# Kernel optimization log

Hardware: AMD Instinct MI355X
Metric: run time of the kernel (lower is better)

## Reference

```python
import jax, jax.numpy as jnp
import numpy as np

H = 64  # GRU hidden size


def _gru_layer(x, Wih, Whh, bih, bhh):
    """PyTorch-semantics GRU layer. x: [B,T,I] -> [B,T,H].
    r = sig(Wir x + bir + Whr h + bhr); z = sig(...); n = tanh(Win x + bin + r*(Whn h + bhn))
    h' = (1-z)*n + z*h. Gate order in stacked weights: r, z, n."""
    xg = jnp.einsum('bti,gi->btg', x, Wih) + bih  # [B,T,3H], precomputed input projections

    def step(h, xg_t):
        hg = h @ Whh.T + bhh  # [B,3H]
        xr, xz, xn = jnp.split(xg_t, 3, axis=-1)
        hr, hz, hn = jnp.split(hg, 3, axis=-1)
        r = jax.nn.sigmoid(xr + hr)
        z = jax.nn.sigmoid(xz + hz)
        n = jnp.tanh(xn + r * hn)
        h_new = (1.0 - z) * n + z * h
        return h_new, h_new

    h0 = jnp.zeros((x.shape[0], H), x.dtype)
    _, ys = jax.lax.scan(step, h0, jnp.swapaxes(xg, 0, 1))  # scan over time
    return jnp.swapaxes(ys, 0, 1)  # [B,T,H]


def _gru_stack4(x, Wih0, Wih, Whh, bih, bhh):
    # layer 0 has its own input width; layers 1..3 take H->H. Inter-layer dropout
    # (p=0.2) is inference-disabled.
    y = _gru_layer(x, Wih0, Whh[0], bih[0], bhh[0])
    for l in range(3):
        y = _gru_layer(y, Wih[l], Whh[l + 1], bih[l + 1], bhh[l + 1])
    return y


def _bn_eval(x, gamma, beta, mean, var, eps=1e-5):
    return gamma * (x - mean) * jax.lax.rsqrt(var + eps) + beta


def setup_inputs() -> dict:
    key = jax.random.key(0)
    ks = jax.random.split(key, 32)
    B, T = 2048, 256
    d = {}
    d['sentiment_seq'] = jax.random.normal(ks[0], (B, T), jnp.float32)
    d['price_seq'] = jax.random.normal(ks[1], (B, T, 4), jnp.float32)
    w = lambda k, s: jax.random.normal(k, s, jnp.float32) * 0.1
    d['s_Wih0'] = w(ks[2], (192, 1)); d['s_Wih'] = w(ks[3], (3, 192, 64))
    d['s_Whh'] = w(ks[4], (4, 192, 64)); d['s_bih'] = w(ks[5], (4, 192)); d['s_bhh'] = w(ks[6], (4, 192))
    d['p_Wih0'] = w(ks[7], (192, 4)); d['p_Wih'] = w(ks[8], (3, 192, 64))
    d['p_Whh'] = w(ks[9], (4, 192, 64)); d['p_bih'] = w(ks[10], (4, 192)); d['p_bhh'] = w(ks[11], (4, 192))
    d['fc1_W'] = w(ks[12], (128, 128)); d['fc1_b'] = w(ks[13], (128,))
    d['bn1_gamma'] = jax.random.uniform(ks[14], (128,), jnp.float32, 0.5, 1.5)
    d['bn1_beta'] = w(ks[15], (128,)); d['bn1_mean'] = w(ks[16], (128,))
    d['bn1_var'] = jax.random.uniform(ks[17], (128,), jnp.float32, 0.5, 1.5)
    d['fc2_W'] = w(ks[18], (128, 128)); d['fc2_b'] = w(ks[19], (128,))
    d['bn2_gamma'] = jax.random.uniform(ks[20], (128,), jnp.float32, 0.5, 1.5)
    d['bn2_beta'] = w(ks[21], (128,)); d['bn2_mean'] = w(ks[22], (128,))
    d['bn2_var'] = jax.random.uniform(ks[23], (128,), jnp.float32, 0.5, 1.5)
    d['fc3_W'] = w(ks[24], (2, 128)); d['fc3_b'] = w(ks[25], (2,))
    return d


def reference(sentiment_seq, price_seq,
              s_Wih0, s_Wih, s_Whh, s_bih, s_bhh,
              p_Wih0, p_Wih, p_Whh, p_bih, p_bhh,
              fc1_W, fc1_b, bn1_gamma, bn1_beta, bn1_mean, bn1_var,
              fc2_W, fc2_b, bn2_gamma, bn2_beta, bn2_mean, bn2_var,
              fc3_W, fc3_b):
    # input_size[0] == 1 -> unsqueeze last dim (as in the torch module)
    s = sentiment_seq[..., None]                         # [B,T,1]
    s_out = _gru_stack4(s, s_Wih0, s_Wih, s_Whh, s_bih, s_bhh)
    p_out = _gru_stack4(price_seq, p_Wih0, p_Wih, p_Whh, p_bih, p_bhh)
    x = jnp.concatenate([s_out[:, -1, :], p_out[:, -1, :]], axis=1)  # [B,128]
    x = x @ fc1_W.T + fc1_b
    x = jax.nn.relu(_bn_eval(x, bn1_gamma, bn1_beta, bn1_mean, bn1_var))  # dropout off (eval)
    x = x @ fc2_W.T + fc2_b
    x = jax.nn.relu(_bn_eval(x, bn2_gamma, bn2_beta, bn2_mean, bn2_var))
    return x @ fc3_W.T + fc3_b  # [B,2] logits
```

## Files before the change

### kernel.cpp

```cpp
#include <hip/hip_runtime.h>

namespace {

constexpr int BB = 2048;
constexpr int TT = 256;
constexpr float L2E = 1.4426950408889634f;

typedef __attribute__((ext_vector_type(8))) short bf8;
typedef __attribute__((ext_vector_type(4))) float f4;
typedef __attribute__((ext_vector_type(2))) unsigned int u32x2;

#define MFMA16(a, b, c) __builtin_amdgcn_mfma_f32_16x16x32_bf16((a), (b), (c), 0, 0, 0)

__device__ __forceinline__ unsigned short f2bf_rne(float f) {
  unsigned int x = __float_as_uint(f);
  return (unsigned short)((x + 0x7fffu + ((x >> 16) & 1u)) >> 16);
}
__device__ __forceinline__ void mk_hilo(float v, short& hi, short& lo) {
  unsigned int u = __float_as_uint(v);
  hi = (short)(u >> 16);
  float r = v - __uint_as_float(u & 0xffff0000u);
  lo = (short)(__float_as_uint(r) >> 16);
}

__device__ __forceinline__ void waitq(const unsigned* c, unsigned tgt) {
  while (__hip_atomic_load(c, __ATOMIC_ACQUIRE, __HIP_MEMORY_SCOPE_WORKGROUP) < tgt) {}
}

__global__ __launch_bounds__(1024, 4) void gru_all(
    const float* __restrict__ xs, const float* __restrict__ xp,
    const float* __restrict__ W0s, const float* __restrict__ W0p,
    const float* __restrict__ Wihs, const float* __restrict__ Wihp,
    const float* __restrict__ Whhs, const float* __restrict__ Whhp,
    const float* __restrict__ bihs, const float* __restrict__ bihp,
    const float* __restrict__ bhhs, const float* __restrict__ bhhp,
    float* __restrict__ hlast) {
  const int tid = threadIdx.x;
  const int Wv = tid >> 6, lane = tid & 63;
  const int g = Wv >> 2, w = Wv & 3;
  const int n15 = lane & 15, q = lane >> 4;
  const int blk = blockIdx.x, stack = blk >> 7;
  const int b0 = (blk & 127) * 16;

  const float* Wh = (stack ? Whhp : Whhs) + (size_t)g * 192 * 64;
  const float* bi = (stack ? bihp : bihs) + g * 192;
  const float* bh = (stack ? bhhp : bhhs) + g * 192;
  const float* Wx = (stack ? Wihp : Wihs) + (size_t)(g - 1) * 192 * 64;

  __shared__ unsigned short hb[4][4][8][16][8];
  __shared__ unsigned qdone[4];

  for (int e = tid; e < 4 * 4 * 8 * 16 * 8; e += 1024)
    ((unsigned short*)hb)[e] = 0;
  if (tid < 4) qdone[tid] = 0;
  __syncthreads();

  const int mrow = 16 * w + n15;
  const int mu = 16 * w + 4 * q;
  const int fr_w = 2 * w + (q >> 1);
  const int eo_w = (q & 1) * 4;

  const float gsc[3] = {L2E, L2E, 2.f * L2E};

  bf8 whh_[3][2];
  #pragma unroll
  for (int i = 0; i < 3; ++i) {
    #pragma unroll
    for (int kt = 0; kt < 2; ++kt) {
      const float* ph_ = Wh + (size_t)(i * 64 + mrow) * 64 + kt * 32 + q * 8;
      f4 ha = *(const f4*)ph_, hc = *(const f4*)(ph_ + 4);
      bf8 h2;
      #pragma unroll
      for (int j = 0; j < 8; ++j)
        h2[j] = (short)f2bf_rne(gsc[i] * ((j < 4) ? ha[j] : hc[j - 4]));
      whh_[i][kt] = h2;
    }
  }
  bf8 wxh_[3][2];
  if (g >= 1) {
    #pragma unroll
    for (int i = 0; i < 3; ++i) {
      #pragma unroll
      for (int kt = 0; kt < 2; ++kt) {
        const float* px_ = Wx + (size_t)(i * 64 + mrow) * 64 + kt * 32 + q * 8;
        f4 xa = *(const f4*)px_, xc = *(const f4*)(px_ + 4);
        bf8 h1;
        #pragma unroll
        for (int j = 0; j < 8; ++j)
          h1[j] = (short)f2bf_rne(gsc[i] * ((j < 4) ? xa[j] : xc[j - 4]));
        wxh_[i][kt] = h1;
      }
    }
  } else {
    const float* W0 = stack ? W0p : W0s;
    #pragma unroll
    for (int i = 0; i < 3; ++i) {
      bf8 a;
      #pragma unroll
      for (int j = 0; j < 8; ++j) a[j] = 0;
      if (q == 0) {
        if (stack) {
          #pragma unroll
          for (int d = 0; d < 4; ++d) {
            short hi, lo;
            mk_hilo(gsc[i] * W0[(size_t)(i * 64 + mrow) * 4 + d], hi, lo);
            a[d] = hi; a[4 + d] = lo;
          }
        } else {
          short hi, lo; mk_hilo(gsc[i] * W0[i * 64 + mrow], hi, lo);
          a[0] = hi; a[1] = hi; a[4] = lo; a[5] = lo;
        }
      }
      wxh_[i][0] = a; wxh_[i][1] = a;
    }
  }

  f4 bR, bZ, bNx, bNh;
  #pragma unroll
  for (int r = 0; r < 4; ++r) {
    bR[r]  = L2E * (bi[mu + r] + bh[mu + r]);
    bZ[r]  = L2E * (bi[64 + mu + r] + bh[64 + mu + r]);
    bNx[r] = 2.f * L2E * bi[128 + mu + r];
    bNh[r] = 2.f * L2E * bh[128 + mu + r];
  }
  f4 h = {0.f, 0.f, 0.f, 0.f};

  const size_t xrow = (size_t)(b0 + n15);
  float px0 = 0.f, px1 = 0.f, px2 = 0.f, px3 = 0.f;
  if (g == 0) {
    if (stack) { f4 t4 = *(const f4*)(xp + xrow * TT * 4); px0 = t4[0]; px1 = t4[1]; px2 = t4[2]; px3 = t4[3]; }
    else       { px0 = xs[xrow * TT]; }
  }

#define GRU_BODY(S)                                                            \
  {                                                                            \
    constexpr int SW = (S + 1) & 3;                                            \
    f4 aR = bR, aZ = bZ, aNx = bNx, aNh = bNh;                                 \
    if (g == 0) {                                                              \
      bf8 xq;                                                                  \
      _Pragma("unroll") for (int j = 0; j < 8; ++j) xq[j] = 0;                 \
      if (q == 0) {                                                            \
        if (stack) {                                                           \
          short a0 = (short)f2bf_rne(px0), a1 = (short)f2bf_rne(px1);          \
          short a2 = (short)f2bf_rne(px2), a3 = (short)f2bf_rne(px3);          \
          xq[0] = a0; xq[1] = a1; xq[2] = a2; xq[3] = a3;                      \
          xq[4] = a0; xq[5] = a1; xq[6] = a2; xq[7] = a3;                      \
        } else {                                                               \
          unsigned short xh = f2bf_rne(px0);                                   \
          float xf = __uint_as_float((unsigned)xh << 16);                      \
          unsigned short xl = f2bf_rne(px0 - xf);                              \
          xq[0] = (short)xh; xq[1] = (short)xl;                                \
          xq[4] = (short)xh; xq[5] = (short)xl;                                \
        }                                                                      \
      }                                                                        \
      __builtin_amdgcn_s_setprio(1);                                           \
      aR  = MFMA16(wxh_[0][0], xq, aR);                                        \
      aZ  = MFMA16(wxh_[1][0], xq, aZ);                                        \
      aNx = MFMA16(wxh_[2][0], xq, aNx);                                       \
      __builtin_amdgcn_s_setprio(0);                                           \
      if (tc + 1 < TT) {                                                       \
        if (stack) { f4 t4 = *(const f4*)(xp + (xrow * TT + tc + 1) * 4);      \
                     px0 = t4[0]; px1 = t4[1]; px2 = t4[2]; px3 = t4[3]; }     \
        else       { px0 = xs[xrow * TT + tc + 1]; }                           \
      }                                                                        \
    } else {                                                                   \
      waitq(&qdone[g - 1], 4u * (unsigned)(tc + 1));                           \
      bf8 xc0 = *(const bf8*)&hb[g - 1][SW][q][n15][0];                        \
      bf8 xc1 = *(const bf8*)&hb[g - 1][SW][4 + q][n15][0];                    \
      __builtin_amdgcn_s_setprio(1);                                           \
      aR  = MFMA16(wxh_[0][0], xc0, aR);  aR  = MFMA16(wxh_[0][1], xc1, aR);   \
      aZ  = MFMA16(wxh_[1][0], xc0, aZ);  aZ  = MFMA16(wxh_[1][1], xc1, aZ);   \
      aNx = MFMA16(wxh_[2][0], xc0, aNx); aNx = MFMA16(wxh_[2][1], xc1, aNx);  \
      __builtin_amdgcn_s_setprio(0);                                           \
    }                                                                          \
    waitq(&qdone[g], 4u * (unsigned)tc);                                       \
    bf8 hh0 = *(const bf8*)&hb[g][S][q][n15][0];                               \
    bf8 hh1 = *(const bf8*)&hb[g][S][4 + q][n15][0];                           \
    __builtin_amdgcn_s_setprio(1);                                             \
    aR  = MFMA16(whh_[0][0], hh0, aR);  aR  = MFMA16(whh_[0][1], hh1, aR);     \
    aZ  = MFMA16(whh_[1][0], hh0, aZ);  aZ  = MFMA16(whh_[1][1], hh1, aZ);     \
    aNh = MFMA16(whh_[2][0], hh0, aNh); aNh = MFMA16(whh_[2][1], hh1, aNh);    \
    __builtin_amdgcn_s_setprio(0);                                             \
    if (g < 3 && tc >= 4) waitq(&qdone[g + 1], 4u * (unsigned)(tc - 3));       \
    _Pragma("unroll") for (int r = 0; r < 4; ++r) {                            \
      float eR = __builtin_amdgcn_exp2f(-aR[r]);                               \
      float eZ = __builtin_amdgcn_exp2f(-aZ[r]);                               \
      float dR = 1.f + eR, dZ = 1.f + eZ;                                      \
      float qq = __builtin_amdgcn_rcpf(dR * dZ);                               \
      float rr = dZ * qq;                            \
      float zz = dR * qq;                            \
      float eN = __builtin_amdgcn_exp2f(aNx[r] + rr * aNh[r]);                 \
      float nn = 1.f - 2.f * __builtin_amdgcn_rcpf(eN + 1.f);                  \
      h[r] = nn + zz * (h[r] - nn);                                            \
    }                                                                          \
    unsigned p01, p23;                                                         \
    asm("v_cvt_pk_bf16_f32 %0, %1, %2" : "=v"(p01) : "v"(h[0]), "v"(h[1]));   \
    asm("v_cvt_pk_bf16_f32 %0, %1, %2" : "=v"(p23) : "v"(h[2]), "v"(h[3]));   \
    u32x2 hiw = {p01, p23};                                                    \
    *(u32x2*)&hb[g][SW][fr_w][n15][eo_w] = hiw;                                \
    if (g == 3 && tc == TT - 1)                                                \
      *(f4*)&hlast[((size_t)stack * BB + b0 + n15) * 64 + mu] = h;             \
    if (lane == 0)                                                             \
      __hip_atomic_fetch_add(&qdone[g], 1u, __ATOMIC_RELEASE,                  \
                             __HIP_MEMORY_SCOPE_WORKGROUP);                    \
  }

  for (int t = 0; t < TT; t += 4) {
    { const int tc = t;     GRU_BODY(0) }
    { const int tc = t + 1; GRU_BODY(1) }
    { const int tc = t + 2; GRU_BODY(2) }
    { const int tc = t + 3; GRU_BODY(3) }
  }
#undef GRU_BODY
}

__global__ __launch_bounds__(128) void head(
    const float* __restrict__ hlast,
    const float* __restrict__ W1, const float* __restrict__ b1,
    const float* __restrict__ g1, const float* __restrict__ be1,
    const float* __restrict__ m1, const float* __restrict__ v1,
    const float* __restrict__ W2, const float* __restrict__ b2,
    const float* __restrict__ g2, const float* __restrict__ be2,
    const float* __restrict__ m2, const float* __restrict__ v2,
    const float* __restrict__ W3, const float* __restrict__ b3,
    float* __restrict__ out) {
  const int b = blockIdx.x;
  const int j = threadIdx.x;
  __shared__ float xin[128];
  __shared__ float y1[128];
  __shared__ float y2[128];
  xin[j] = (j < 64) ? hlast[(size_t)b * 64 + j]
                    : hlast[(size_t)BB * 64 + (size_t)b * 64 + (j - 64)];
  __syncthreads();
  float acc = b1[j];
  #pragma unroll 8
  for (int k = 0; k < 128; ++k) acc = fmaf(W1[j * 128 + k], xin[k], acc);
  float sc = g1[j] * rsqrtf(v1[j] + 1e-5f);
  y1[j] = fmaxf(0.f, (acc - m1[j]) * sc + be1[j]);
  __syncthreads();
  acc = b2[j];
  #pragma unroll 8
  for (int k = 0; k < 128; ++k) acc = fmaf(W2[j * 128 + k], y1[k], acc);
  sc = g2[j] * rsqrtf(v2[j] + 1e-5f);
  y2[j] = fmaxf(0.f, (acc - m2[j]) * sc + be2[j]);
  __syncthreads();
  if (j < 2) {
    float a = b3[j];
    #pragma unroll 8
    for (int k = 0; k < 128; ++k) a = fmaf(W3[j * 128 + k], y2[k], a);
    out[(size_t)b * 2 + j] = a;
  }
}

}

extern "C" void kernel_launch(void* const* d_in, const int* in_sizes, int n_in,
                              void* d_out, int out_size, void* d_ws, size_t ws_size,
                              hipStream_t stream) {
  (void)in_sizes; (void)n_in; (void)out_size; (void)ws_size;
  const float* sent   = (const float*)d_in[0];
  const float* price  = (const float*)d_in[1];
  const float* s_Wih0 = (const float*)d_in[2];
  const float* s_Wih  = (const float*)d_in[3];
  const float* s_Whh  = (const float*)d_in[4];
  const float* s_bih  = (const float*)d_in[5];
  const float* s_bhh  = (const float*)d_in[6];
  const float* p_Wih0 = (const float*)d_in[7];
  const float* p_Wih  = (const float*)d_in[8];
  const float* p_Whh  = (const float*)d_in[9];
  const float* p_bih  = (const float*)d_in[10];
  const float* p_bhh  = (const float*)d_in[11];
  const float* fc1_W  = (const float*)d_in[12];
  const float* fc1_b  = (const float*)d_in[13];
  const float* bn1_g  = (const float*)d_in[14];
  const float* bn1_b  = (const float*)d_in[15];
  const float* bn1_m  = (const float*)d_in[16];
  const float* bn1_v  = (const float*)d_in[17];
  const float* fc2_W  = (const float*)d_in[18];
  const float* fc2_b  = (const float*)d_in[19];
  const float* bn2_g  = (const float*)d_in[20];
  const float* bn2_b  = (const float*)d_in[21];
  const float* bn2_m  = (const float*)d_in[22];
  const float* bn2_v  = (const float*)d_in[23];
  const float* fc3_W  = (const float*)d_in[24];
  const float* fc3_b  = (const float*)d_in[25];
  float* out = (float*)d_out;

  float* hlast = (float*)d_ws;

  gru_all<<<dim3(256), dim3(1024), 0, stream>>>(
      sent, price, s_Wih0, p_Wih0, s_Wih, p_Wih, s_Whh, p_Whh,
      s_bih, p_bih, s_bhh, p_bhh, hlast);

  head<<<dim3(BB), dim3(128), 0, stream>>>(
      hlast, fc1_W, fc1_b, bn1_g, bn1_b, bn1_m, bn1_v,
      fc2_W, fc2_b, bn2_g, bn2_b, bn2_m, bn2_v, fc3_W, fc3_b, out);
}
```

Before: 282.5 us.

## Replace per-layer atomic spin-waits with diagonal wavefront schedule and block barriers

The four GRU layers in a block no longer use LDS atomic counters and spin-waits to hand hidden states between layers. They now run on a diagonal schedule: at global step s, layer g processes time s-g, with one __syncthreads per step, and the ring-buffer slot pointers are precomputed per unrolled phase. This removes atomic polling traffic on LDS and the per-step release/acquire handshakes. In exchange all 16 waves move in lockstep, so the slack the counter scheme allowed between layers is lost, and there are three extra pipeline fill/drain steps.

After: 283.7 us. Within noise of the previous version (+0.4%).

```diff
diff --git a/kernel.cpp b/kernel.cpp
--- a/kernel.cpp
+++ b/kernel.cpp
@@ -21,10 +21,6 @@
   hi = (short)(u >> 16);
   float r = v - __uint_as_float(u & 0xffff0000u);
   lo = (short)(__float_as_uint(r) >> 16);
-}
-
-__device__ __forceinline__ void waitq(const unsigned* c, unsigned tgt) {
-  while (__hip_atomic_load(c, __ATOMIC_ACQUIRE, __HIP_MEMORY_SCOPE_WORKGROUP) < tgt) {}
 }
 
 __global__ __launch_bounds__(1024, 4) void gru_all(
@@ -48,12 +44,9 @@
   const float* Wx = (stack ? Wihp : Wihs) + (size_t)(g - 1) * 192 * 64;
 
   __shared__ unsigned short hb[4][4][8][16][8];
-  __shared__ unsigned qdone[4];
 
   for (int e = tid; e < 4 * 4 * 8 * 16 * 8; e += 1024)
     ((unsigned short*)hb)[e] = 0;
-  if (tid < 4) qdone[tid] = 0;
-  __syncthreads();
 
   const int mrow = 16 * w + n15;
   const int mu = 16 * w + 4 * q;
@@ -125,91 +118,102 @@
   }
   f4 h = {0.f, 0.f, 0.f, 0.f};
 
+  const unsigned short* rs0[4];
+  const unsigned short* rp0[4];
+  unsigned short* ws0[4];
+  #pragma unroll
+  for (int j = 0; j < 4; ++j) {
+    const int s_self = (j - g) & 3;
+    const int s_next = (j - g + 1) & 3;
+    rs0[j] = &hb[g][s_self][q][n15][0];
+    ws0[j] = &hb[g][s_next][fr_w][n15][eo_w];
+    rp0[j] = &hb[(g >= 1 ? g - 1 : 0)][s_next][q][n15][0];
+  }
+
   const size_t xrow = (size_t)(b0 + n15);
   float px0 = 0.f, px1 = 0.f, px2 = 0.f, px3 = 0.f;
   if (g == 0) {
     if (stack) { f4 t4 = *(const f4*)(xp + xrow * TT * 4); px0 = t4[0]; px1 = t4[1]; px2 = t4[2]; px3 = t4[3]; }
     else       { px0 = xs[xrow * TT]; }
   }
+  __syncthreads();
 
 #define GRU_BODY(S)                                                            \
   {                                                                            \
-    constexpr int SW = (S + 1) & 3;                                            \
-    f4 aR = bR, aZ = bZ, aNx = bNx, aNh = bNh;                                 \
-    if (g == 0) {                                                              \
-      bf8 xq;                                                                  \
-      _Pragma("unroll") for (int j = 0; j < 8; ++j) xq[j] = 0;                 \
-      if (q == 0) {                                                            \
-        if (stack) {                                                           \
-          short a0 = (short)f2bf_rne(px0), a1 = (short)f2bf_rne(px1);          \
-          short a2 = (short)f2bf_rne(px2), a3 = (short)f2bf_rne(px3);          \
-          xq[0] = a0; xq[1] = a1; xq[2] = a2; xq[3] = a3;                      \
-          xq[4] = a0; xq[5] = a1; xq[6] = a2; xq[7] = a3;                      \
-        } else {                                                               \
-          unsigned short xh = f2bf_rne(px0);                                   \
-          float xf = __uint_as_float((unsigned)xh << 16);                      \
-          unsigned short xl = f2bf_rne(px0 - xf);                              \
-          xq[0] = (short)xh; xq[1] = (short)xl;                                \
-          xq[4] = (short)xh; xq[5] = (short)xl;                                \
+    const int tc = s + S - g;                                                  \
+    if ((unsigned)tc < (unsigned)TT) {                                         \
+      f4 aR = bR, aZ = bZ, aNx = bNx, aNh = bNh;                               \
+      bf8 hh0 = *(const bf8*)rs0[S];                                           \
+      bf8 hh1 = *(const bf8*)(rs0[S] + 512);                                   \
+      if (g == 0) {                                                            \
+        bf8 xq;                                                                \
+        _Pragma("unroll") for (int j = 0; j < 8; ++j) xq[j] = 0;               \
+        if (q == 0) {                                                          \
+          if (stack) {                                                         \
+            short a0 = (short)f2bf_rne(px0), a1 = (short)f2bf_rne(px1);        \
+            short a2 = (short)f2bf_rne(px2), a3 = (short)f2bf_rne(px3);        \
+            xq[0] = a0; xq[1] = a1; xq[2] = a2; xq[3] = a3;                    \
+            xq[4] = a0; xq[5] = a1; xq[6] = a2; xq[7] = a3;                    \
+          } else {                                                             \
+            unsigned short xh = f2bf_rne(px0);                                 \
+            float xf = __uint_as_float((unsigned)xh << 16);                    \
+            unsigned short xl = f2bf_rne(px0 - xf);                            \
+            xq[0] = (short)xh; xq[1] = (short)xl;                              \
+            xq[4] = (short)xh; xq[5] = (short)xl;                              \
+          }                                                                    \
         }                                                                      \
+        __builtin_amdgcn_s_setprio(1);                                         \
+        aR  = MFMA16(wxh_[0][0], xq, aR);                                      \
+        aZ  = MFMA16(wxh_[1][0], xq, aZ);                                      \
+        aNx = MFMA16(wxh_[2][0], xq, aNx);                                     \
+        aR  = MFMA16(whh_[0][0], hh0, aR);  aR  = MFMA16(whh_[0][1], hh1, aR); \
+        aZ  = MFMA16(whh_[1][0], hh0, aZ);  aZ  = MFMA16(whh_[1][1], hh1, aZ); \
+        aNh = MFMA16(whh_[2][0], hh0, aNh); aNh = MFMA16(whh_[2][1], hh1, aNh);\
+        __builtin_amdgcn_s_setprio(0);                                         \
+        if (tc + 1 < TT) {                                                     \
+          if (stack) { f4 t4 = *(const f4*)(xp + (xrow * TT + tc + 1) * 4);    \
+                       px0 = t4[0]; px1 = t4[1]; px2 = t4[2]; px3 = t4[3]; }   \
+          else       { px0 = xs[xrow * TT + tc + 1]; }                         \
+        }                                                                      \
+      } else {                                                                 \
+        bf8 xc0 = *(const bf8*)rp0[S];                                         \
+        bf8 xc1 = *(const bf8*)(rp0[S] + 512);                                 \
+        __builtin_amdgcn_s_setprio(1);                                         \
+        aR  = MFMA16(wxh_[0][0], xc0, aR);  aR  = MFMA16(wxh_[0][1], xc1, aR); \
+        aZ  = MFMA16(wxh_[1][0], xc0, aZ);  aZ  = MFMA16(wxh_[1][1], xc1, aZ); \
+        aNx = MFMA16(wxh_[2][0], xc0, aNx); aNx = MFMA16(wxh_[2][1], xc1, aNx);\
+        aR  = MFMA16(whh_[0][0], hh0, aR);  aR  = MFMA16(whh_[0][1], hh1, aR); \
+        aZ  = MFMA16(whh_[1][0], hh0, aZ);  aZ  = MFMA16(whh_[1][1], hh1, aZ); \
+        aNh = MFMA16(whh_[2][0], hh0, aNh); aNh = MFMA16(whh_[2][1], hh1, aNh);\
+        __builtin_amdgcn_s_setprio(0);                                         \
       }                                                                        \
-      __builtin_amdgcn_s_setprio(1);                                           \
-      aR  = MFMA16(wxh_[0][0], xq, aR);                                        \
-      aZ  = MFMA16(wxh_[1][0], xq, aZ);                                        \
-      aNx = MFMA16(wxh_[2][0], xq, aNx);                                       \
-      __builtin_amdgcn_s_setprio(0);                                           \
-      if (tc + 1 < TT) {                                                       \
-        if (stack) { f4 t4 = *(const f4*)(xp + (xrow * TT + tc + 1) * 4);      \
-                     px0 = t4[0]; px1 = t4[1]; px2 = t4[2]; px3 = t4[3]; }     \
-        else       { px0 = xs[xrow * TT + tc + 1]; }                           \
+      _Pragma("unroll") for (int r = 0; r < 4; ++r) {                          \
+        float eR = __builtin_amdgcn_exp2f(-aR[r]);                             \
+        float eZ = __builtin_amdgcn_exp2f(-aZ[r]);                             \
+        float dR = 1.f + eR, dZ = 1.f + eZ;                                    \
+        float qq = __builtin_amdgcn_rcpf(dR * dZ);                             \
+        float rr = dZ * qq;                                   \
+        float zz = dR * qq;                                   \
+        float eN = __builtin_amdgcn_exp2f(aNx[r] + rr * aNh[r]);               \
+        float nn = 1.f - 2.f * __builtin_amdgcn_rcpf(eN + 1.f);                \
+        h[r] = nn + zz * (h[r] - nn);                                          \
       }                                                                        \
-    } else {                                                                   \
-      waitq(&qdone[g - 1], 4u * (unsigned)(tc + 1));                           \
-      bf8 xc0 = *(const bf8*)&hb[g - 1][SW][q][n15][0];                        \
-      bf8 xc1 = *(const bf8*)&hb[g - 1][SW][4 + q][n15][0];                    \
-      __builtin_amdgcn_s_setprio(1);                                           \
-      aR  = MFMA16(wxh_[0][0], xc0, aR);  aR  = MFMA16(wxh_[0][1], xc1, aR);   \
-      aZ  = MFMA16(wxh_[1][0], xc0, aZ);  aZ  = MFMA16(wxh_[1][1], xc1, aZ);   \
-      aNx = MFMA16(wxh_[2][0], xc0, aNx); aNx = MFMA16(wxh_[2][1], xc1, aNx);  \
-      __builtin_amdgcn_s_setprio(0);                                           \
+      unsigned p01, p23;                                                       \
+      asm("v_cvt_pk_bf16_f32 %0, %1, %2" : "=v"(p01) : "v"(h[0]), "v"(h[1])); \
+      asm("v_cvt_pk_bf16_f32 %0, %1, %2" : "=v"(p23) : "v"(h[2]), "v"(h[3])); \
+      u32x2 hiw = {p01, p23};                                                  \
+      *(u32x2*)ws0[S] = hiw;                                                   \
+      if (g == 3 && tc == TT - 1)                                              \
+        *(f4*)&hlast[((size_t)stack * BB + b0 + n15) * 64 + mu] = h;           \
     }                                                                          \
-    waitq(&qdone[g], 4u * (unsigned)tc);                                       \
-    bf8 hh0 = *(const bf8*)&hb[g][S][q][n15][0];                               \
-    bf8 hh1 = *(const bf8*)&hb[g][S][4 + q][n15][0];                           \
-    __builtin_amdgcn_s_setprio(1);                                             \
-    aR  = MFMA16(whh_[0][0], hh0, aR);  aR  = MFMA16(whh_[0][1], hh1, aR);     \
-    aZ  = MFMA16(whh_[1][0], hh0, aZ);  aZ  = MFMA16(whh_[1][1], hh1, aZ);     \
-    aNh = MFMA16(whh_[2][0], hh0, aNh); aNh = MFMA16(whh_[2][1], hh1, aNh);    \
-    __builtin_amdgcn_s_setprio(0);                                             \
-    if (g < 3 && tc >= 4) waitq(&qdone[g + 1], 4u * (unsigned)(tc - 3));       \
-    _Pragma("unroll") for (int r = 0; r < 4; ++r) {                            \
-      float eR = __builtin_amdgcn_exp2f(-aR[r]);                               \
-      float eZ = __builtin_amdgcn_exp2f(-aZ[r]);                               \
-      float dR = 1.f + eR, dZ = 1.f + eZ;                                      \
-      float qq = __builtin_amdgcn_rcpf(dR * dZ);                               \
-      float rr = dZ * qq;                            \
-      float zz = dR * qq;                            \
-      float eN = __builtin_amdgcn_exp2f(aNx[r] + rr * aNh[r]);                 \
-      float nn = 1.f - 2.f * __builtin_amdgcn_rcpf(eN + 1.f);                  \
-      h[r] = nn + zz * (h[r] - nn);                                            \
-    }                                                                          \
-    unsigned p01, p23;                                                         \
-    asm("v_cvt_pk_bf16_f32 %0, %1, %2" : "=v"(p01) : "v"(h[0]), "v"(h[1]));   \
-    asm("v_cvt_pk_bf16_f32 %0, %1, %2" : "=v"(p23) : "v"(h[2]), "v"(h[3]));   \
-    u32x2 hiw = {p01, p23};                                                    \
-    *(u32x2*)&hb[g][SW][fr_w][n15][eo_w] = hiw;                                \
-    if (g == 3 && tc == TT - 1)                                                \
-      *(f4*)&hlast[((size_t)stack * BB + b0 + n15) * 64 + mu] = h;             \
-    if (lane == 0)                                                             \
-      __hip_atomic_fetch_add(&qdone[g], 1u, __ATOMIC_RELEASE,                  \
-                             __HIP_MEMORY_SCOPE_WORKGROUP);                    \
-  }
-
-  for (int t = 0; t < TT; t += 4) {
-    { const int tc = t;     GRU_BODY(0) }
-    { const int tc = t + 1; GRU_BODY(1) }
-    { const int tc = t + 2; GRU_BODY(2) }
-    { const int tc = t + 3; GRU_BODY(3) }
+    __syncthreads();                                                           \
+  }
+
+  for (int s = 0; s < TT + 4; s += 4) {
+    GRU_BODY(0)
+    GRU_BODY(1)
+    GRU_BODY(2)
+    GRU_BODY(3)
   }
 #undef GRU_BODY
 }
```
